# Optimization experiments

Hardware: AMD Instinct MI355X
Metric: run time of the kernel (lower is better)

Reference implementation:

```python
import jax, jax.numpy as jnp
import numpy as np

N, E, G = 50000, 640000, 256
NODE_IN, EDGE_IN, EXT_IN = 32, 16, 8
H, L = 128, 3
BN_EPS = 1e-5


def _linear_init(key, fan_in, fan_out):
    kw, kb = jax.random.split(key)
    s = 1.0 / np.sqrt(fan_in)
    w = jax.random.uniform(kw, (fan_in, fan_out), minval=-s, maxval=s, dtype=jnp.float32)
    b = jax.random.uniform(kb, (fan_out,), minval=-s, maxval=s, dtype=jnp.float32)
    return w, b


def setup_inputs() -> dict:
    key = jax.random.key(0)
    ks = jax.random.split(key, 16)
    x = jax.random.normal(ks[0], (N, NODE_IN), dtype=jnp.float32)
    edge_index = jax.random.randint(ks[1], (2, E), 0, N)
    edge_attr = jax.random.normal(ks[2], (E, EDGE_IN), dtype=jnp.float32)
    batch = jnp.sort(jax.random.randint(ks[3], (N,), 0, G))
    externals = jax.random.normal(ks[4], (G, EXT_IN), dtype=jnp.float32)

    node_w, node_b = _linear_init(ks[5], NODE_IN, H)
    ee_w1, ee_b1 = _linear_init(ks[6], EDGE_IN, H)
    ee_w2, ee_b2 = _linear_init(ks[7], H, H)
    # stacked per-layer GINEConv MLP params: [L, H, H] / [L, H]
    cks = jax.random.split(ks[8], 2 * L)
    cw1, cb1, cw2, cb2 = [], [], [], []
    for l in range(L):
        w1, b1 = _linear_init(cks[2 * l], H, H)
        w2, b2 = _linear_init(cks[2 * l + 1], H, H)
        cw1.append(w1); cb1.append(b1); cw2.append(w2); cb2.append(b2)
    conv_w1 = jnp.stack(cw1); conv_b1 = jnp.stack(cb1)
    conv_w2 = jnp.stack(cw2); conv_b2 = jnp.stack(cb2)
    bn_gamma = jnp.ones((L, H), dtype=jnp.float32)
    bn_beta = jnp.zeros((L, H), dtype=jnp.float32)
    ext_w1, ext_b1 = _linear_init(ks[9], EXT_IN, H)
    ext_w2, ext_b2 = _linear_init(ks[10], H, H)
    reg_w1, reg_b1 = _linear_init(ks[11], 2 * H, H)
    reg_w2, reg_b2 = _linear_init(ks[12], H, 1)

    return dict(x=x, edge_attr=edge_attr, externals=externals,
                node_w=node_w, node_b=node_b,
                ee_w1=ee_w1, ee_b1=ee_b1, ee_w2=ee_w2, ee_b2=ee_b2,
                conv_w1=conv_w1, conv_b1=conv_b1, conv_w2=conv_w2, conv_b2=conv_b2,
                bn_gamma=bn_gamma, bn_beta=bn_beta,
                ext_w1=ext_w1, ext_b1=ext_b1, ext_w2=ext_w2, ext_b2=ext_b2,
                reg_w1=reg_w1, reg_b1=reg_b1, reg_w2=reg_w2, reg_b2=reg_b2,
                edge_index=edge_index, batch=batch, num_graphs=G)


def reference(x, edge_attr, externals,
              node_w, node_b, ee_w1, ee_b1, ee_w2, ee_b2,
              conv_w1, conv_b1, conv_w2, conv_b2, bn_gamma, bn_beta,
              ext_w1, ext_b1, ext_w2, ext_b2,
              reg_w1, reg_b1, reg_w2, reg_b2,
              edge_index, batch, num_graphs):
    n = x.shape[0]
    src, dst = edge_index[0], edge_index[1]
    h = x @ node_w + node_b                                      # [N,H]
    e = jax.nn.relu(edge_attr @ ee_w1 + ee_b1) @ ee_w2 + ee_b2   # [E,H]
    for l in range(conv_w1.shape[0]):
        # GINEConv (eps=0): aggr = sum_j relu(x_j + e_ij); out = MLP(x_i + aggr)
        msg = jax.nn.relu(h[src] + e)                            # gather + add + relu [E,H]
        aggr = jax.ops.segment_sum(msg, dst, num_segments=n)     # scatter-add [N,H]
        z = h + aggr
        z = jax.nn.relu(z @ conv_w1[l] + conv_b1[l]) @ conv_w2[l] + conv_b2[l]
        # BatchNorm1d (batch statistics)
        mean = z.mean(axis=0)
        var = z.var(axis=0)
        z = (z - mean) * jax.lax.rsqrt(var + BN_EPS) * bn_gamma[l] + bn_beta[l]
        h = jax.nn.relu(z)                                       # dropout = identity (eval)
    # global mean pool over graphs
    gsum = jax.ops.segment_sum(h, batch, num_segments=num_graphs)
    cnt = jax.ops.segment_sum(jnp.ones((n, 1), h.dtype), batch, num_segments=num_graphs)
    graph_emb = gsum / jnp.maximum(cnt, 1.0)
    ext = jax.nn.relu(externals @ ext_w1 + ext_b1) @ ext_w2 + ext_b2
    comb = jnp.concatenate([graph_emb, ext], axis=-1)            # [G,2H]
    out = jax.nn.relu(comb @ reg_w1 + reg_b1) @ reg_w2 + reg_b2  # [G,1]
    return out.squeeze(-1)
```

## Files before the change

kernel.cpp:

```cpp
#include <hip/hip_runtime.h>

typedef __bf16 bf16_t;
typedef __bf16 bf16x8 __attribute__((ext_vector_type(8)));
typedef __bf16 bf16x4 __attribute__((ext_vector_type(4)));
typedef __bf16 bf16x2 __attribute__((ext_vector_type(2)));
typedef float  f32x4  __attribute__((ext_vector_type(4)));

#define MFMA16(a, b, c) __builtin_amdgcn_mfma_f32_16x16x32_bf16((a), (b), (c), 0, 0, 0)

__global__ __launch_bounds__(256) void prep_all_kernel(
    const float* __restrict__ nw,  const float* __restrict__ ew1,
    const float* __restrict__ ew2, const float* __restrict__ cw1,
    const float* __restrict__ cw2,
    bf16_t* __restrict__ nwt,  bf16_t* __restrict__ ew1t,
    bf16_t* __restrict__ ew2t, bf16_t* __restrict__ cw1t,
    bf16_t* __restrict__ cw2t)
{
    int b = blockIdx.x;
    const float* W; bf16_t* O; int Kact, KP, lb;
    if (b < 16)       { W = nw;  O = nwt;  Kact = 32;  KP = 32;  lb = b; }
    else if (b < 32)  { W = ew1; O = ew1t; Kact = 16;  KP = 32;  lb = b - 16; }
    else if (b < 96)  { W = ew2; O = ew2t; Kact = 128; KP = 128; lb = b - 32; }
    else if (b < 288) { int l = (b - 96) / 64;  W = cw1 + l * 16384; O = cw1t + l * 16384;
                        Kact = 128; KP = 128; lb = (b - 96) % 64; }
    else              { int l = (b - 288) / 64; W = cw2 + l * 16384; O = cw2t + l * 16384;
                        Kact = 128; KP = 128; lb = (b - 288) % 64; }
    int idx = lb * 256 + threadIdx.x;
    if (idx >= 128 * KP) return;
    int j    = idx & 7;
    int lane = (idx >> 3) & 63;
    int ct   = (idx >> 9) & 7;
    int kc   = idx >> 12;
    int n = ct * 16 + (lane & 15);
    int k = kc * 32 + (lane >> 4) * 8 + j;
    O[idx] = (bf16_t)((k < Kact) ? W[k * 128 + n] : 0.0f);
}

__global__ __launch_bounds__(256) void hist_kernel(const int* __restrict__ ei,
                                                   int* __restrict__ deg, int E,
                                                   const float* __restrict__ ea) {
    int t = blockIdx.x * 256 + threadIdx.x;
    if (t < E) {
        atomicAdd(&deg[ei[(long)E + t]], 1);
        float w0 = ea[(long)t * 16];
        float w1 = ea[(long)t * 16 + 8];
        asm volatile("" :: "v"(w0), "v"(w1));
    }
}

__global__ __launch_bounds__(256) void scanA_kernel(const int* __restrict__ deg,
                                                    int* __restrict__ partials,
                                                    int* __restrict__ bsums, int N) {
    __shared__ int s[256];
    int b = blockIdx.x, t = threadIdx.x;
    int base = b * 1024 + t * 4;
    int v0 = (base + 0 < N) ? deg[base + 0] : 0;
    int v1 = (base + 1 < N) ? deg[base + 1] : 0;
    int v2 = (base + 2 < N) ? deg[base + 2] : 0;
    int v3 = (base + 3 < N) ? deg[base + 3] : 0;
    int local = v0 + v1 + v2 + v3;
    s[t] = local;
    __syncthreads();
    for (int off = 1; off < 256; off <<= 1) {
        int v = (t >= off) ? s[t - off] : 0;
        __syncthreads();
        s[t] += v;
        __syncthreads();
    }
    int excl = s[t] - local;
    if (base + 0 < N) partials[base + 0] = excl;
    if (base + 1 < N) partials[base + 1] = excl + v0;
    if (base + 2 < N) partials[base + 2] = excl + v0 + v1;
    if (base + 3 < N) partials[base + 3] = excl + v0 + v1 + v2;
    if (t == 255) bsums[b] = s[255];
}

__global__ __launch_bounds__(256) void scanB_kernel(const int* __restrict__ bsums,
                                                    int* __restrict__ boff,
                                                    int* __restrict__ rowptr,
                                                    int NB, int N) {
    __shared__ int s[256];
    int t = threadIdx.x;
    int local = (t < NB) ? bsums[t] : 0;
    s[t] = local;
    __syncthreads();
    for (int off = 1; off < 256; off <<= 1) {
        int v = (t >= off) ? s[t - off] : 0;
        __syncthreads();
        s[t] += v;
        __syncthreads();
    }
    if (t < NB) boff[t] = s[t] - local;
    if (t == NB - 1) rowptr[N] = s[t];
}

__global__ __launch_bounds__(256) void scanC_kernel(const int* __restrict__ partials,
                                                    const int* __restrict__ boff,
                                                    int* __restrict__ rowptr,
                                                    int* __restrict__ cursor, int N) {
    int i = blockIdx.x * 256 + threadIdx.x;
    if (i >= N) return;
    int v = partials[i] + boff[i >> 10];
    rowptr[i] = v;
    cursor[i] = v;
}

__global__ __launch_bounds__(256) void scatter_kernel(const int* __restrict__ ei,
                                                      int* __restrict__ cursor,
                                                      int* __restrict__ srcp,
                                                      int* __restrict__ epos, int E) {
    int t = blockIdx.x * 256 + threadIdx.x;
    if (t >= E) return;
    int d = ei[(long)E + t];
    int pos = atomicAdd(&cursor[d], 1);
    srcp[pos] = ei[t];
    epos[t] = pos;
}

__global__ __launch_bounds__(256) void node_enc_kernel(
    const float* __restrict__ A, int M,
    const bf16_t* __restrict__ Ws, const float* __restrict__ bias,
    bf16_t* __restrict__ outp)
{
    constexpr int S = 136;
    __shared__ bf16_t T[128 * S];

    const int  tid  = threadIdx.x;
    const int  wv   = tid >> 6, lane = tid & 63;
    const long row0 = (long)blockIdx.x * 128;
    const int  l16  = lane & 15, quad = lane >> 4;

    {
        int r  = wv * 32 + (lane >> 1);
        long gr = row0 + r;
        int c0 = (lane & 1) * 16;
#pragma unroll
        for (int q = 0; q < 4; ++q) {
            float4 v = make_float4(0.f, 0.f, 0.f, 0.f);
            if (gr < M) v = *(const float4*)(A + gr * 32 + c0 + q * 4);
            bf16_t* d = &T[r * S + c0 + q * 4];
            d[0] = (bf16_t)v.x; d[1] = (bf16_t)v.y; d[2] = (bf16_t)v.z; d[3] = (bf16_t)v.w;
        }
    }

    f32x4 acc[2][8];
#pragma unroll
    for (int r = 0; r < 2; r++)
#pragma unroll
        for (int c = 0; c < 8; c++) acc[r][c] = (f32x4){0.f, 0.f, 0.f, 0.f};

    {
        bf16x8 af0 = *(const bf16x8*)&T[(wv * 32 + l16) * S + quad * 8];
        bf16x8 af1 = *(const bf16x8*)&T[(wv * 32 + 16 + l16) * S + quad * 8];
#pragma unroll
        for (int c = 0; c < 8; c++) {
            bf16x8 bfr = *(const bf16x8*)&Ws[((c * 64) + lane) * 8];
            acc[0][c] = MFMA16(af0, bfr, acc[0][c]);
            acc[1][c] = MFMA16(af1, bfr, acc[1][c]);
        }
    }

#pragma unroll
    for (int r = 0; r < 2; r++) {
        int mrow = wv * 32 + r * 16 + quad * 4;
#pragma unroll
        for (int c = 0; c < 8; c++) {
            int col = c * 16 + l16;
            float bb = bias[col];
#pragma unroll
            for (int q = 0; q < 4; q++)
                T[(mrow + q) * S + col] = (bf16_t)(acc[r][c][q] + bb);
        }
    }

#pragma unroll
    for (int it = 0; it < 8; ++it) {
        int idx = it * 64 + lane;
        int row = wv * 32 + (idx >> 4);
        int seg = idx & 15;
        long grow = row0 + row;
        if (grow < M)
            *(uint4*)&outp[grow * 128 + seg * 8] = *(const uint4*)&T[row * S + seg * 8];
    }
}

__global__ __launch_bounds__(256) void edge_mlp_kernel(
    const float* __restrict__ A, int M,
    const bf16_t* __restrict__ Ws1, const float* __restrict__ b1,
    const bf16_t* __restrict__ Ws2, const float* __restrict__ b2,
    const int* __restrict__ epos, bf16_t* __restrict__ outp)
{
    constexpr int S = 136;
    __shared__ bf16_t T[64 * S];

    const int  tid  = threadIdx.x;
    const int  wv   = tid >> 6, lane = tid & 63;
    const long row0 = (long)blockIdx.x * 64;
    const int  l16  = lane & 15, quad = lane >> 4;

    {
        int  r  = wv * 16 + (lane >> 2);
        long gr = row0 + r;
        float4 v = make_float4(0.f, 0.f, 0.f, 0.f);
        if (gr < M) v = *(const float4*)(A + gr * 16 + (lane & 3) * 4);
        bf16_t* d = &T[r * S + (lane & 3) * 4];
        d[0] = (bf16_t)v.x; d[1] = (bf16_t)v.y; d[2] = (bf16_t)v.z; d[3] = (bf16_t)v.w;
    }

    f32x4 acc[8];
#pragma unroll
    for (int c = 0; c < 8; c++) acc[c] = (f32x4){0.f, 0.f, 0.f, 0.f};

    {
        bf16x8 af;
#pragma unroll
        for (int j = 0; j < 8; ++j) af[j] = (bf16_t)0.f;
        if (quad < 2) af = *(const bf16x8*)&T[(wv * 16 + l16) * S + quad * 8];
#pragma unroll
        for (int c = 0; c < 8; c++) {
            bf16x8 bfr = *(const bf16x8*)&Ws1[((c * 64) + lane) * 8];
            acc[c] = MFMA16(af, bfr, acc[c]);
        }
    }

    const int mbase = wv * 16 + quad * 4;

#pragma unroll
    for (int c = 0; c < 8; c++) {
        int col = c * 16 + l16;
        float bb = b1[col];
#pragma unroll
        for (int q = 0; q < 4; q++)
            T[(mbase + q) * S + col] = (bf16_t)fmaxf(acc[c][q] + bb, 0.f);
    }

#pragma unroll
    for (int c = 0; c < 8; c++) acc[c] = (f32x4){0.f, 0.f, 0.f, 0.f};

#pragma unroll
    for (int kc = 0; kc < 4; ++kc) {
        bf16x8 af = *(const bf16x8*)&T[(wv * 16 + l16) * S + kc * 32 + quad * 8];
#pragma unroll
        for (int c = 0; c < 8; c++) {
            bf16x8 bfr = *(const bf16x8*)&Ws2[(((kc * 8 + c) * 64) + lane) * 8];
            acc[c] = MFMA16(af, bfr, acc[c]);
        }
    }

#pragma unroll
    for (int c = 0; c < 8; c++) {
        int col = c * 16 + l16;
        float bb = b2[col];
#pragma unroll
        for (int q = 0; q < 4; q++)
            T[(mbase + q) * S + col] = (bf16_t)(acc[c][q] + bb);
    }

#pragma unroll
    for (int it = 0; it < 4; ++it) {
        int idx = it * 64 + lane;
        int row = wv * 16 + (idx >> 4);
        int seg = idx & 15;
        long grow = row0 + row;
        if (grow < M) {
            long pos = epos[grow];
            *(uint4*)&outp[pos * 128 + seg * 8] = *(const uint4*)&T[row * S + seg * 8];
        }
    }
}

__global__ __launch_bounds__(256) void bnx_kernel(
    const bf16_t* __restrict__ z, const float* __restrict__ bns,
    const float* __restrict__ gamma, const float* __restrict__ beta,
    bf16_t* __restrict__ hbuf, int N)
{
    long t = (long)blockIdx.x * 256 + threadIdx.x;
    long i0 = t * 8;
    if (i0 >= (long)N * 128) return;
    int c = (int)(i0 & 127);
    const float invN = 1.f / (float)N;
    bf16x8 v = *(const bf16x8*)(z + i0);
    bf16x8 o;
#pragma unroll
    for (int u = 0; u < 8; ++u) {
        int cc = c + u;
        float m  = bns[cc] * invN;
        float va = bns[128 + cc] * invN - m * m;
        float iv = rsqrtf(va + 1e-5f);
        float sc = gamma[cc] * iv;
        float sh = beta[cc] - m * sc;
        o[u] = (bf16_t)fmaxf((float)v[u] * sc + sh, 0.f);
    }
    *(bf16x8*)(hbuf + i0) = o;
}

__global__ __launch_bounds__(512, 8) void aggr_conv_kernel(
    const bf16_t* __restrict__ xin,
    const bf16_t* __restrict__ e,
    const int* __restrict__ rowptr, const int* __restrict__ srcp, int M,
    const bf16_t* __restrict__ Ws1, const float* __restrict__ b1,
    const bf16_t* __restrict__ Ws2, const float* __restrict__ b2,
    bf16_t* __restrict__ zout, float* __restrict__ bn_out)
{
    constexpr int S = 136;
    __shared__ bf16_t T[32 * S];
    __shared__ float  wred[2][256];

    const int  tid  = threadIdx.x;
    const int  wv   = tid >> 6, lane = tid & 63;
    const long row0 = (long)blockIdx.x * 32;
    const int  l16  = lane & 15, quad = lane >> 4;

    const long nbase = row0 + wv * 4;
    int rpv = 0;
    {
        long idx = nbase + lane;
        if (idx > M) idx = M;
        if (lane <= 4) rpv = rowptr[idx];
    }

#pragma unroll 1
    for (int ri = 0; ri < 4; ++ri) {
        const int  r   = wv * 4 + ri;
        const long n   = row0 + r;
        const int  beg = __shfl(rpv, ri);
        const int  end = __shfl(rpv, ri + 1);
        float ax = 0.f, ay = 0.f;
        if (n < M) {
            bf16x2 xv = *(const bf16x2*)(xin + n * 128 + lane * 2);
            ax = (float)xv[0]; ay = (float)xv[1];
            for (int base = beg; base < end; base += 64) {
                int cnt = min(64, end - base);
                int sv  = (base + lane < end) ? srcp[base + lane] : 0;
                int j = 0;
                for (; j + 3 < cnt; j += 4) {
                    int s0 = __shfl(sv, j),     s1 = __shfl(sv, j + 1);
                    int s2 = __shfl(sv, j + 2), s3 = __shfl(sv, j + 3);
                    bf16x2 x0 = *(const bf16x2*)(xin + (long)s0 * 128 + lane * 2);
                    bf16x2 x1 = *(const bf16x2*)(xin + (long)s1 * 128 + lane * 2);
                    bf16x2 x2 = *(const bf16x2*)(xin + (long)s2 * 128 + lane * 2);
                    bf16x2 x3 = *(const bf16x2*)(xin + (long)s3 * 128 + lane * 2);
                    bf16x2 e0 = *(const bf16x2*)(e + (long)(base + j + 0) * 128 + lane * 2);
                    bf16x2 e1 = *(const bf16x2*)(e + (long)(base + j + 1) * 128 + lane * 2);
                    bf16x2 e2 = *(const bf16x2*)(e + (long)(base + j + 2) * 128 + lane * 2);
                    bf16x2 e3 = *(const bf16x2*)(e + (long)(base + j + 3) * 128 + lane * 2);
                    ax += fmaxf((float)x0[0] + (float)e0[0], 0.f);
                    ay += fmaxf((float)x0[1] + (float)e0[1], 0.f);
                    ax += fmaxf((float)x1[0] + (float)e1[0], 0.f);
                    ay += fmaxf((float)x1[1] + (float)e1[1], 0.f);
                    ax += fmaxf((float)x2[0] + (float)e2[0], 0.f);
                    ay += fmaxf((float)x2[1] + (float)e2[1], 0.f);
                    ax += fmaxf((float)x3[0] + (float)e3[0], 0.f);
                    ay += fmaxf((float)x3[1] + (float)e3[1], 0.f);
                }
                for (; j < cnt; ++j) {
                    int s0 = __shfl(sv, j);
                    bf16x2 x0 = *(const bf16x2*)(xin + (long)s0 * 128 + lane * 2);
                    bf16x2 e0 = *(const bf16x2*)(e + (long)(base + j) * 128 + lane * 2);
                    ax += fmaxf((float)x0[0] + (float)e0[0], 0.f);
                    ay += fmaxf((float)x0[1] + (float)e0[1], 0.f);
                }
            }
        }
        bf16x2 o; o[0] = (bf16_t)ax; o[1] = (bf16_t)ay;
        *(bf16x2*)&T[r * S + lane * 2] = o;
    }
    __syncthreads();

    const int rb = wv >> 2, cq = wv & 3;
    const int mbase = rb * 16 + quad * 4;

    f32x4 acc[2];
#pragma unroll
    for (int c = 0; c < 2; c++) acc[c] = (f32x4){0.f, 0.f, 0.f, 0.f};

#pragma unroll
    for (int kc = 0; kc < 4; ++kc) {
        bf16x8 af = *(const bf16x8*)&T[(rb * 16 + l16) * S + kc * 32 + quad * 8];
#pragma unroll
        for (int c = 0; c < 2; c++) {
            int ct = cq * 2 + c;
            bf16x8 bfr = *(const bf16x8*)&Ws1[(((kc * 8 + ct) * 64) + lane) * 8];
            acc[c] = MFMA16(af, bfr, acc[c]);
        }
    }
    __syncthreads();

#pragma unroll
    for (int c = 0; c < 2; c++) {
        int col = (cq * 2 + c) * 16 + l16;
        float bb = b1[col];
#pragma unroll
        for (int q = 0; q < 4; q++)
            T[(mbase + q) * S + col] = (bf16_t)fmaxf(acc[c][q] + bb, 0.f);
    }
    __syncthreads();

#pragma unroll
    for (int c = 0; c < 2; c++) acc[c] = (f32x4){0.f, 0.f, 0.f, 0.f};

#pragma unroll
    for (int kc = 0; kc < 4; ++kc) {
        bf16x8 af = *(const bf16x8*)&T[(rb * 16 + l16) * S + kc * 32 + quad * 8];
#pragma unroll
        for (int c = 0; c < 2; c++) {
            int ct = cq * 2 + c;
            bf16x8 bfr = *(const bf16x8*)&Ws2[(((kc * 8 + ct) * 64) + lane) * 8];
            acc[c] = MFMA16(af, bfr, acc[c]);
        }
    }
    __syncthreads();

#pragma unroll
    for (int c = 0; c < 2; c++) {
        int col = (cq * 2 + c) * 16 + l16;
        float bb = b2[col];
        float s = 0.f, s2 = 0.f;
#pragma unroll
        for (int q = 0; q < 4; q++) {
            float v = acc[c][q] + bb;
            T[(mbase + q) * S + col] = (bf16_t)v;
            if (row0 + mbase + q < M) { s += v; s2 += v * v; }
        }
        s  += __shfl_xor(s, 16);  s  += __shfl_xor(s, 32);
        s2 += __shfl_xor(s2, 16); s2 += __shfl_xor(s2, 32);
        if (quad == 0) {
            wred[rb][col]       = s;
            wred[rb][128 + col] = s2;
        }
    }
    __syncthreads();

    {
        int row = tid >> 4, seg = tid & 15;
        long grow = row0 + row;
        if (grow < M)
            *(uint4*)&zout[grow * 128 + seg * 8] = *(const uint4*)&T[row * S + seg * 8];
    }
    if (tid < 256) {
        float v = wred[0][tid] + wred[1][tid];
        atomicAdd(&bn_out[tid], v);
    }
}

__global__ __launch_bounds__(128) void pool_kernel(
    const bf16_t* __restrict__ z, const float* __restrict__ bns,
    const float* __restrict__ gamma, const float* __restrict__ beta,
    const int* __restrict__ batch,
    float* __restrict__ gsum, float* __restrict__ cnt, int N)
{
    int c = threadIdx.x;
    float mean = bns[c] / (float)N;
    float var  = bns[128 + c] / (float)N - mean * mean;
    float inv  = rsqrtf(var + 1e-5f);
    float sc   = gamma[c] * inv;
    float sh   = beta[c] - mean * sc;
    int n0 = blockIdx.x * 32;
    int n1 = min(n0 + 32, N);
    float acc = 0.f;
    int cur = -1, rc = 0;
    for (int n = n0; n < n1; ++n) {
        int g = batch[n];
        if (g != cur) {
            if (cur >= 0) {
                atomicAdd(&gsum[(long)cur * 128 + c], acc);
                if (c == 0) atomicAdd(&cnt[cur], (float)rc);
            }
            cur = g; acc = 0.f; rc = 0;
        }
        acc += fmaxf((float)z[(long)n * 128 + c] * sc + sh, 0.f);
        rc++;
    }
    if (cur >= 0) {
        atomicAdd(&gsum[(long)cur * 128 + c], acc);
        if (c == 0) atomicAdd(&cnt[cur], (float)rc);
    }
}

__global__ __launch_bounds__(128) void head_kernel(
    const float* __restrict__ gsum, const float* __restrict__ cnt,
    const float* __restrict__ ext_in,
    const float* __restrict__ ew1, const float* __restrict__ eb1,
    const float* __restrict__ ew2, const float* __restrict__ eb2,
    const float* __restrict__ rw1, const float* __restrict__ rb1,
    const float* __restrict__ rw2, const float* __restrict__ rb2,
    float* __restrict__ out)
{
    int g = blockIdx.x, c = threadIdx.x;
    __shared__ float sx[8];
    __shared__ float h1[128];
    __shared__ float comb[256];
    __shared__ float red[128];

    if (c < 8) sx[c] = ext_in[g * 8 + c];
    __syncthreads();
    float a = eb1[c];
#pragma unroll
    for (int k = 0; k < 8; k++) a += sx[k] * ew1[k * 128 + c];
    h1[c] = fmaxf(a, 0.f);
    __syncthreads();
    float b = eb2[c];
    for (int k = 0; k < 128; k++) b += h1[k] * ew2[k * 128 + c];
    comb[c]       = gsum[(long)g * 128 + c] / fmaxf(cnt[g], 1.0f);
    comb[128 + c] = b;
    __syncthreads();
    float r = rb1[c];
    for (int k = 0; k < 256; k++) r += comb[k] * rw1[k * 128 + c];
    r = fmaxf(r, 0.f);
    red[c] = r * rw2[c];
    __syncthreads();
    if (c == 0) {
        float s = rb2[0];
        for (int k = 0; k < 128; k++) s += red[k];
        out[g] = s;
    }
}

extern "C" void kernel_launch(void* const* d_in, const int* in_sizes, int n_in,
                              void* d_out, int out_size, void* d_ws, size_t ws_size,
                              hipStream_t stream)
{
    const float* x         = (const float*)d_in[0];
    const float* edge_attr = (const float*)d_in[1];
    const float* externals = (const float*)d_in[2];
    const float* node_w    = (const float*)d_in[3];
    const float* node_b    = (const float*)d_in[4];
    const float* ee_w1     = (const float*)d_in[5];
    const float* ee_b1     = (const float*)d_in[6];
    const float* ee_w2     = (const float*)d_in[7];
    const float* ee_b2     = (const float*)d_in[8];
    const float* conv_w1   = (const float*)d_in[9];
    const float* conv_b1   = (const float*)d_in[10];
    const float* conv_w2   = (const float*)d_in[11];
    const float* conv_b2   = (const float*)d_in[12];
    const float* bn_gamma  = (const float*)d_in[13];
    const float* bn_beta   = (const float*)d_in[14];
    const float* ext_w1    = (const float*)d_in[15];
    const float* ext_b1    = (const float*)d_in[16];
    const float* ext_w2    = (const float*)d_in[17];
    const float* ext_b2    = (const float*)d_in[18];
    const float* reg_w1    = (const float*)d_in[19];
    const float* reg_b1    = (const float*)d_in[20];
    const float* reg_w2    = (const float*)d_in[21];
    const float* reg_b2    = (const float*)d_in[22];
    const int* edge_index  = (const int*)d_in[23];
    const int* batch       = (const int*)d_in[24];

    const int N = in_sizes[0] / 32;
    const int E = in_sizes[1] / 16;
    const int G = in_sizes[2] / 8;
    const int NB = (N + 1023) / 1024;

    char* p = (char*)d_ws;
    auto alloc = [&](size_t bytes) -> void* {
        void* r = (void*)p;
        p += (bytes + 255) & ~(size_t)255;
        return r;
    };
    bf16_t* h       = (bf16_t*)alloc((size_t)N * 128 * 2);
    bf16_t* zA      = (bf16_t*)alloc((size_t)N * 128 * 2);
    bf16_t* zB      = (bf16_t*)alloc((size_t)N * 128 * 2);
    bf16_t* hb      = (bf16_t*)alloc((size_t)N * 128 * 2);
    bf16_t* ebuf    = (bf16_t*)alloc((size_t)E * 128 * 2);
    int*    deg     = (int*)alloc((size_t)N * 4);
    int*    rowptr  = (int*)alloc(((size_t)N + 1) * 4);
    int*    cursor  = (int*)alloc((size_t)N * 4);
    int*    partials= (int*)alloc((size_t)N * 4);
    int*    bsums   = (int*)alloc((size_t)NB * 4);
    int*    boff    = (int*)alloc((size_t)NB * 4);
    int*    srcp    = (int*)alloc((size_t)E * 4);
    int*    epos    = (int*)alloc((size_t)E * 4);
    bf16_t* node_wt = (bf16_t*)alloc(128 * 32 * 2);
    bf16_t* ee_w1t  = (bf16_t*)alloc(128 * 32 * 2);
    bf16_t* ee_w2t  = (bf16_t*)alloc(128 * 128 * 2);
    bf16_t* cw1t    = (bf16_t*)alloc(3 * 128 * 128 * 2);
    bf16_t* cw2t    = (bf16_t*)alloc(3 * 128 * 128 * 2);
    float*  bns     = (float*)alloc(3 * 256 * 4);
    float*  gsum    = (float*)alloc((size_t)G * 128 * 4);
    float*  cnt     = (float*)alloc((size_t)G * 4);

    hipMemsetAsync(deg, 0, (size_t)N * 4, stream);
    hipMemsetAsync(bns, 0, 3 * 256 * 4, stream);
    hist_kernel<<<(E + 255) / 256, 256, 0, stream>>>(edge_index, deg, E, edge_attr);
    scanA_kernel<<<NB, 256, 0, stream>>>(deg, partials, bsums, N);
    scanB_kernel<<<1, 256, 0, stream>>>(bsums, boff, rowptr, NB, N);
    scanC_kernel<<<(N + 255) / 256, 256, 0, stream>>>(partials, boff, rowptr, cursor, N);
    scatter_kernel<<<(E + 255) / 256, 256, 0, stream>>>(edge_index, cursor, srcp, epos, E);

    prep_all_kernel<<<480, 256, 0, stream>>>(node_w, ee_w1, ee_w2, conv_w1, conv_w2,
                                             node_wt, ee_w1t, ee_w2t, cw1t, cw2t);

    node_enc_kernel<<<(N + 127) / 128, 256, 0, stream>>>(x, N, node_wt, node_b, h);

    edge_mlp_kernel<<<(E + 63) / 64, 256, 0, stream>>>(
        edge_attr, E, ee_w1t, ee_b1, ee_w2t, ee_b2, epos, ebuf);

    const int nblk = (N + 31) / 32;
    const int bblk = ((N * 128 / 8) + 255) / 256;
    aggr_conv_kernel<<<nblk, 512, 0, stream>>>(
        h, ebuf, rowptr, srcp, N,
        cw1t + 0 * 16384, conv_b1 + 0 * 128, cw2t + 0 * 16384, conv_b2 + 0 * 128,
        zA, bns + 0);
    bnx_kernel<<<bblk, 256, 0, stream>>>(zA, bns + 0, bn_gamma + 0, bn_beta + 0, hb, N);
    aggr_conv_kernel<<<nblk, 512, 0, stream>>>(
        hb, ebuf, rowptr, srcp, N,
        cw1t + 1 * 16384, conv_b1 + 1 * 128, cw2t + 1 * 16384, conv_b2 + 1 * 128,
        zB, bns + 256);
    bnx_kernel<<<bblk, 256, 0, stream>>>(zB, bns + 256, bn_gamma + 128, bn_beta + 128, hb, N);
    aggr_conv_kernel<<<nblk, 512, 0, stream>>>(
        hb, ebuf, rowptr, srcp, N,
        cw1t + 2 * 16384, conv_b1 + 2 * 128, cw2t + 2 * 16384, conv_b2 + 2 * 128,
        zA, bns + 512);

    hipMemsetAsync(gsum, 0, (size_t)G * 128 * 4, stream);
    hipMemsetAsync(cnt, 0, (size_t)G * 4, stream);
    pool_kernel<<<(N + 31) / 32, 128, 0, stream>>>(zA, bns + 512, bn_gamma + 256, bn_beta + 256,
                                                   batch, gsum, cnt, N);
    head_kernel<<<G, 128, 0, stream>>>(gsum, cnt, externals,
                                       ext_w1, ext_b1, ext_w2, ext_b2,
                                       reg_w1, reg_b1, reg_w2, reg_b2,
                                       (float*)d_out);
}
```

Measured before the change: 549.5 us.

## Stage edge features via async global-to-LDS loads and batch 16 neighbor gathers

Result: slower. 594.7 us (+8.2%).

```diff
diff --git a/kernel.cpp b/kernel.cpp
--- a/kernel.cpp
+++ b/kernel.cpp
@@ -7,6 +7,9 @@
 typedef float  f32x4  __attribute__((ext_vector_type(4)));
 
 #define MFMA16(a, b, c) __builtin_amdgcn_mfma_f32_16x16x32_bf16((a), (b), (c), 0, 0, 0)
+
+typedef __attribute__((address_space(1))) const void gvoid_t;
+typedef __attribute__((address_space(3))) void svoid_t;
 
 __global__ __launch_bounds__(256) void prep_all_kernel(
     const float* __restrict__ nw,  const float* __restrict__ ew1,
@@ -294,7 +297,7 @@
     *(bf16x8*)(hbuf + i0) = o;
 }
 
-__global__ __launch_bounds__(512, 8) void aggr_conv_kernel(
+__global__ __launch_bounds__(512, 6) void aggr_conv_kernel(
     const bf16_t* __restrict__ xin,
     const bf16_t* __restrict__ e,
     const int* __restrict__ rowptr, const int* __restrict__ srcp, int M,
@@ -305,11 +308,14 @@
     constexpr int S = 136;
     __shared__ bf16_t T[32 * S];
     __shared__ float  wred[2][256];
+    __shared__ bf16_t Elds[8][16 * 128];
 
     const int  tid  = threadIdx.x;
     const int  wv   = tid >> 6, lane = tid & 63;
     const long row0 = (long)blockIdx.x * 32;
     const int  l16  = lane & 15, quad = lane >> 4;
+
+    bf16_t* eslot = &Elds[wv][0];
 
     const long nbase = row0 + wv * 4;
     int rpv = 0;
@@ -327,39 +333,51 @@
         const int  end = __shfl(rpv, ri + 1);
         float ax = 0.f, ay = 0.f;
         if (n < M) {
-            bf16x2 xv = *(const bf16x2*)(xin + n * 128 + lane * 2);
-            ax = (float)xv[0]; ay = (float)xv[1];
-            for (int base = beg; base < end; base += 64) {
-                int cnt = min(64, end - base);
-                int sv  = (base + lane < end) ? srcp[base + lane] : 0;
-                int j = 0;
-                for (; j + 3 < cnt; j += 4) {
-                    int s0 = __shfl(sv, j),     s1 = __shfl(sv, j + 1);
-                    int s2 = __shfl(sv, j + 2), s3 = __shfl(sv, j + 3);
-                    bf16x2 x0 = *(const bf16x2*)(xin + (long)s0 * 128 + lane * 2);
-                    bf16x2 x1 = *(const bf16x2*)(xin + (long)s1 * 128 + lane * 2);
-                    bf16x2 x2 = *(const bf16x2*)(xin + (long)s2 * 128 + lane * 2);
-                    bf16x2 x3 = *(const bf16x2*)(xin + (long)s3 * 128 + lane * 2);
-                    bf16x2 e0 = *(const bf16x2*)(e + (long)(base + j + 0) * 128 + lane * 2);
-                    bf16x2 e1 = *(const bf16x2*)(e + (long)(base + j + 1) * 128 + lane * 2);
-                    bf16x2 e2 = *(const bf16x2*)(e + (long)(base + j + 2) * 128 + lane * 2);
-                    bf16x2 e3 = *(const bf16x2*)(e + (long)(base + j + 3) * 128 + lane * 2);
-                    ax += fmaxf((float)x0[0] + (float)e0[0], 0.f);
-                    ay += fmaxf((float)x0[1] + (float)e0[1], 0.f);
-                    ax += fmaxf((float)x1[0] + (float)e1[0], 0.f);
-                    ay += fmaxf((float)x1[1] + (float)e1[1], 0.f);
-                    ax += fmaxf((float)x2[0] + (float)e2[0], 0.f);
-                    ay += fmaxf((float)x2[1] + (float)e2[1], 0.f);
-                    ax += fmaxf((float)x3[0] + (float)e3[0], 0.f);
-                    ay += fmaxf((float)x3[1] + (float)e3[1], 0.f);
+            bf16x2 xv0 = *(const bf16x2*)(xin + n * 128 + lane * 2);
+            ax = (float)xv0[0]; ay = (float)xv0[1];
+#pragma unroll 1
+            for (int base = beg; base < end; base += 16) {
+                int cnt = min(16, end - base);
+#pragma unroll
+                for (int i = 0; i < 4; ++i) {
+                    __builtin_amdgcn_global_load_lds(
+                        (gvoid_t*)(e + (long)base * 128 + i * 512 + lane * 8),
+                        (svoid_t*)(eslot + i * 512),
+                        16, 0, 0);
                 }
-                for (; j < cnt; ++j) {
-                    int s0 = __shfl(sv, j);
-                    bf16x2 x0 = *(const bf16x2*)(xin + (long)s0 * 128 + lane * 2);
-                    bf16x2 e0 = *(const bf16x2*)(e + (long)(base + j) * 128 + lane * 2);
-                    ax += fmaxf((float)x0[0] + (float)e0[0], 0.f);
-                    ay += fmaxf((float)x0[1] + (float)e0[1], 0.f);
-                }
+                int sv = (lane < 16 && base + lane < end) ? srcp[base + lane] : 0;
+                bf16x2 xr0  = *(const bf16x2*)(xin + (long)__shfl(sv, 0)  * 128 + lane * 2);
+                bf16x2 xr1  = *(const bf16x2*)(xin + (long)__shfl(sv, 1)  * 128 + lane * 2);
+                bf16x2 xr2  = *(const bf16x2*)(xin + (long)__shfl(sv, 2)  * 128 + lane * 2);
+                bf16x2 xr3  = *(const bf16x2*)(xin + (long)__shfl(sv, 3)  * 128 + lane * 2);
+                bf16x2 xr4  = *(const bf16x2*)(xin + (long)__shfl(sv, 4)  * 128 + lane * 2);
+                bf16x2 xr5  = *(const bf16x2*)(xin + (long)__shfl(sv, 5)  * 128 + lane * 2);
+                bf16x2 xr6  = *(const bf16x2*)(xin + (long)__shfl(sv, 6)  * 128 + lane * 2);
+                bf16x2 xr7  = *(const bf16x2*)(xin + (long)__shfl(sv, 7)  * 128 + lane * 2);
+                bf16x2 xr8  = *(const bf16x2*)(xin + (long)__shfl(sv, 8)  * 128 + lane * 2);
+                bf16x2 xr9  = *(const bf16x2*)(xin + (long)__shfl(sv, 9)  * 128 + lane * 2);
+                bf16x2 xr10 = *(const bf16x2*)(xin + (long)__shfl(sv, 10) * 128 + lane * 2);
+                bf16x2 xr11 = *(const bf16x2*)(xin + (long)__shfl(sv, 11) * 128 + lane * 2);
+                bf16x2 xr12 = *(const bf16x2*)(xin + (long)__shfl(sv, 12) * 128 + lane * 2);
+                bf16x2 xr13 = *(const bf16x2*)(xin + (long)__shfl(sv, 13) * 128 + lane * 2);
+                bf16x2 xr14 = *(const bf16x2*)(xin + (long)__shfl(sv, 14) * 128 + lane * 2);
+                bf16x2 xr15 = *(const bf16x2*)(xin + (long)__shfl(sv, 15) * 128 + lane * 2);
+                asm volatile("s_waitcnt vmcnt(0)" ::: "memory");
+                __builtin_amdgcn_sched_barrier(0);
+#define ACC_E(J, XR)                                                           \
+                do {                                                           \
+                    if (J < cnt) {                                             \
+                        bf16x2 ev = *(const bf16x2*)(eslot + J * 128 + lane * 2); \
+                        ax += fmaxf((float)XR[0] + (float)ev[0], 0.f);         \
+                        ay += fmaxf((float)XR[1] + (float)ev[1], 0.f);         \
+                    }                                                          \
+                } while (0)
+                ACC_E(0, xr0);   ACC_E(1, xr1);   ACC_E(2, xr2);   ACC_E(3, xr3);
+                ACC_E(4, xr4);   ACC_E(5, xr5);   ACC_E(6, xr6);   ACC_E(7, xr7);
+                ACC_E(8, xr8);   ACC_E(9, xr9);   ACC_E(10, xr10); ACC_E(11, xr11);
+                ACC_E(12, xr12); ACC_E(13, xr13); ACC_E(14, xr14); ACC_E(15, xr15);
+#undef ACC_E
+                __builtin_amdgcn_sched_barrier(0);
             }
         }
         bf16x2 o; o[0] = (bf16_t)ax; o[1] = (bf16_t)ay;
@@ -561,7 +579,7 @@
     bf16_t* zA      = (bf16_t*)alloc((size_t)N * 128 * 2);
     bf16_t* zB      = (bf16_t*)alloc((size_t)N * 128 * 2);
     bf16_t* hb      = (bf16_t*)alloc((size_t)N * 128 * 2);
-    bf16_t* ebuf    = (bf16_t*)alloc((size_t)E * 128 * 2);
+    bf16_t* ebuf    = (bf16_t*)alloc((size_t)E * 128 * 2 + 8192);
     int*    deg     = (int*)alloc((size_t)N * 4);
     int*    rowptr  = (int*)alloc(((size_t)N + 1) * 4);
     int*    cursor  = (int*)alloc((size_t)N * 4);
```

## Recompute edge MLP inside aggregation kernels instead of materializing edge embeddings

Applied to the files above, without the earlier changes.

Result: slower. 2.081 ms (+278.8%).

```diff
diff --git a/kernel.cpp b/kernel.cpp
--- a/kernel.cpp
+++ b/kernel.cpp
@@ -108,13 +108,18 @@
 __global__ __launch_bounds__(256) void scatter_kernel(const int* __restrict__ ei,
                                                       int* __restrict__ cursor,
                                                       int* __restrict__ srcp,
-                                                      int* __restrict__ epos, int E) {
+                                                      const float* __restrict__ ea,
+                                                      bf16_t* __restrict__ eac, int E) {
     int t = blockIdx.x * 256 + threadIdx.x;
     if (t >= E) return;
     int d = ei[(long)E + t];
     int pos = atomicAdd(&cursor[d], 1);
     srcp[pos] = ei[t];
-    epos[t] = pos;
+    bf16_t tmp[16];
+#pragma unroll
+    for (int k = 0; k < 16; ++k) tmp[k] = (bf16_t)ea[(long)t * 16 + k];
+    *(uint4*)(eac + (long)pos * 16)     = *(uint4*)(tmp);
+    *(uint4*)(eac + (long)pos * 16 + 8) = *(uint4*)(tmp + 8);
 }
 
 __global__ __launch_bounds__(256) void node_enc_kernel(
@@ -181,91 +186,6 @@
         long grow = row0 + row;
         if (grow < M)
             *(uint4*)&outp[grow * 128 + seg * 8] = *(const uint4*)&T[row * S + seg * 8];
-    }
-}
-
-__global__ __launch_bounds__(256) void edge_mlp_kernel(
-    const float* __restrict__ A, int M,
-    const bf16_t* __restrict__ Ws1, const float* __restrict__ b1,
-    const bf16_t* __restrict__ Ws2, const float* __restrict__ b2,
-    const int* __restrict__ epos, bf16_t* __restrict__ outp)
-{
-    constexpr int S = 136;
-    __shared__ bf16_t T[64 * S];
-
-    const int  tid  = threadIdx.x;
-    const int  wv   = tid >> 6, lane = tid & 63;
-    const long row0 = (long)blockIdx.x * 64;
-    const int  l16  = lane & 15, quad = lane >> 4;
-
-    {
-        int  r  = wv * 16 + (lane >> 2);
-        long gr = row0 + r;
-        float4 v = make_float4(0.f, 0.f, 0.f, 0.f);
-        if (gr < M) v = *(const float4*)(A + gr * 16 + (lane & 3) * 4);
-        bf16_t* d = &T[r * S + (lane & 3) * 4];
-        d[0] = (bf16_t)v.x; d[1] = (bf16_t)v.y; d[2] = (bf16_t)v.z; d[3] = (bf16_t)v.w;
-    }
-
-    f32x4 acc[8];
-#pragma unroll
-    for (int c = 0; c < 8; c++) acc[c] = (f32x4){0.f, 0.f, 0.f, 0.f};
-
-    {
-        bf16x8 af;
-#pragma unroll
-        for (int j = 0; j < 8; ++j) af[j] = (bf16_t)0.f;
-        if (quad < 2) af = *(const bf16x8*)&T[(wv * 16 + l16) * S + quad * 8];
-#pragma unroll
-        for (int c = 0; c < 8; c++) {
-            bf16x8 bfr = *(const bf16x8*)&Ws1[((c * 64) + lane) * 8];
-            acc[c] = MFMA16(af, bfr, acc[c]);
-        }
-    }
-
-    const int mbase = wv * 16 + quad * 4;
-
-#pragma unroll
-    for (int c = 0; c < 8; c++) {
-        int col = c * 16 + l16;
-        float bb = b1[col];
-#pragma unroll
-        for (int q = 0; q < 4; q++)
-            T[(mbase + q) * S + col] = (bf16_t)fmaxf(acc[c][q] + bb, 0.f);
-    }
-
-#pragma unroll
-    for (int c = 0; c < 8; c++) acc[c] = (f32x4){0.f, 0.f, 0.f, 0.f};
-
-#pragma unroll
-    for (int kc = 0; kc < 4; ++kc) {
-        bf16x8 af = *(const bf16x8*)&T[(wv * 16 + l16) * S + kc * 32 + quad * 8];
-#pragma unroll
-        for (int c = 0; c < 8; c++) {
-            bf16x8 bfr = *(const bf16x8*)&Ws2[(((kc * 8 + c) * 64) + lane) * 8];
-            acc[c] = MFMA16(af, bfr, acc[c]);
-        }
-    }
-
-#pragma unroll
-    for (int c = 0; c < 8; c++) {
-        int col = c * 16 + l16;
-        float bb = b2[col];
-#pragma unroll
-        for (int q = 0; q < 4; q++)
-            T[(mbase + q) * S + col] = (bf16_t)(acc[c][q] + bb);
-    }
-
-#pragma unroll
-    for (int it = 0; it < 4; ++it) {
-        int idx = it * 64 + lane;
-        int row = wv * 16 + (idx >> 4);
-        int seg = idx & 15;
-        long grow = row0 + row;
-        if (grow < M) {
-            long pos = epos[grow];
-            *(uint4*)&outp[pos * 128 + seg * 8] = *(const uint4*)&T[row * S + seg * 8];
-        }
     }
 }
 
@@ -296,79 +216,146 @@
 
 __global__ __launch_bounds__(512, 8) void aggr_conv_kernel(
     const bf16_t* __restrict__ xin,
-    const bf16_t* __restrict__ e,
+    const bf16_t* __restrict__ eac,
     const int* __restrict__ rowptr, const int* __restrict__ srcp, int M,
+    const bf16_t* __restrict__ We1, const float* __restrict__ be1,
+    const bf16_t* __restrict__ We2, const float* __restrict__ be2,
     const bf16_t* __restrict__ Ws1, const float* __restrict__ b1,
     const bf16_t* __restrict__ Ws2, const float* __restrict__ b2,
     bf16_t* __restrict__ zout, float* __restrict__ bn_out)
 {
     constexpr int S = 136;
-    __shared__ bf16_t T[32 * S];
+    constexpr int STe = 24;
+    __shared__ bf16_t Th[64 * S];
+    __shared__ bf16_t Te[64 * STe];
+    __shared__ float  Acc[32 * 128];
     __shared__ float  wred[2][256];
+    __shared__ int    rptile[33];
+    __shared__ int    dloc[64];
+    __shared__ int    sloc[64];
 
     const int  tid  = threadIdx.x;
     const int  wv   = tid >> 6, lane = tid & 63;
     const long row0 = (long)blockIdx.x * 32;
     const int  l16  = lane & 15, quad = lane >> 4;
 
-    const long nbase = row0 + wv * 4;
-    int rpv = 0;
+    if (tid <= 32) {
+        long idx = row0 + tid;
+        if (idx > M) idx = M;
+        rptile[tid] = rowptr[idx];
+    }
     {
-        long idx = nbase + lane;
-        if (idx > M) idx = M;
-        if (lane <= 4) rpv = rowptr[idx];
-    }
+        int row = tid >> 4;
+        int c0  = (tid & 15) * 8;
+        long n  = row0 + row;
+        if (n < M) {
+            bf16x8 xv = *(const bf16x8*)(xin + n * 128 + c0);
+#pragma unroll
+            for (int u = 0; u < 8; ++u) Acc[row * 128 + c0 + u] = (float)xv[u];
+        } else {
+#pragma unroll
+            for (int u = 0; u < 8; ++u) Acc[row * 128 + c0 + u] = 0.f;
+        }
+    }
+    __syncthreads();
+
+    const int eb = rptile[0];
+    const int ee = rptile[32];
+
+    const int rg = wv >> 1, ch = wv & 1;
+    const int mbase = rg * 16 + quad * 4;
 
 #pragma unroll 1
-    for (int ri = 0; ri < 4; ++ri) {
-        const int  r   = wv * 4 + ri;
-        const long n   = row0 + r;
-        const int  beg = __shfl(rpv, ri);
-        const int  end = __shfl(rpv, ri + 1);
-        float ax = 0.f, ay = 0.f;
-        if (n < M) {
-            bf16x2 xv = *(const bf16x2*)(xin + n * 128 + lane * 2);
-            ax = (float)xv[0]; ay = (float)xv[1];
-            for (int base = beg; base < end; base += 64) {
-                int cnt = min(64, end - base);
-                int sv  = (base + lane < end) ? srcp[base + lane] : 0;
-                int j = 0;
-                for (; j + 3 < cnt; j += 4) {
-                    int s0 = __shfl(sv, j),     s1 = __shfl(sv, j + 1);
-                    int s2 = __shfl(sv, j + 2), s3 = __shfl(sv, j + 3);
-                    bf16x2 x0 = *(const bf16x2*)(xin + (long)s0 * 128 + lane * 2);
-                    bf16x2 x1 = *(const bf16x2*)(xin + (long)s1 * 128 + lane * 2);
-                    bf16x2 x2 = *(const bf16x2*)(xin + (long)s2 * 128 + lane * 2);
-                    bf16x2 x3 = *(const bf16x2*)(xin + (long)s3 * 128 + lane * 2);
-                    bf16x2 e0 = *(const bf16x2*)(e + (long)(base + j + 0) * 128 + lane * 2);
-                    bf16x2 e1 = *(const bf16x2*)(e + (long)(base + j + 1) * 128 + lane * 2);
-                    bf16x2 e2 = *(const bf16x2*)(e + (long)(base + j + 2) * 128 + lane * 2);
-                    bf16x2 e3 = *(const bf16x2*)(e + (long)(base + j + 3) * 128 + lane * 2);
-                    ax += fmaxf((float)x0[0] + (float)e0[0], 0.f);
-                    ay += fmaxf((float)x0[1] + (float)e0[1], 0.f);
-                    ax += fmaxf((float)x1[0] + (float)e1[0], 0.f);
-                    ay += fmaxf((float)x1[1] + (float)e1[1], 0.f);
-                    ax += fmaxf((float)x2[0] + (float)e2[0], 0.f);
-                    ay += fmaxf((float)x2[1] + (float)e2[1], 0.f);
-                    ax += fmaxf((float)x3[0] + (float)e3[0], 0.f);
-                    ay += fmaxf((float)x3[1] + (float)e3[1], 0.f);
-                }
-                for (; j < cnt; ++j) {
-                    int s0 = __shfl(sv, j);
-                    bf16x2 x0 = *(const bf16x2*)(xin + (long)s0 * 128 + lane * 2);
-                    bf16x2 e0 = *(const bf16x2*)(e + (long)(base + j) * 128 + lane * 2);
-                    ax += fmaxf((float)x0[0] + (float)e0[0], 0.f);
-                    ay += fmaxf((float)x0[1] + (float)e0[1], 0.f);
+    for (int cb = eb; cb < ee; cb += 64) {
+        const int cc = min(64, ee - cb);
+        if (tid < 256) {
+            int row = tid >> 2, c4 = (tid & 3) * 4;
+            bf16x4 v = (bf16x4){(bf16_t)0.f, (bf16_t)0.f, (bf16_t)0.f, (bf16_t)0.f};
+            if (row < cc) v = *(const bf16x4*)(eac + (long)(cb + row) * 16 + c4);
+            *(bf16x4*)&Te[row * STe + c4] = v;
+        }
+        if (tid < 64) {
+            sloc[tid] = (tid < cc) ? srcp[cb + tid] : 0;
+            int target = cb + tid;
+            int i = 0;
+#pragma unroll
+            for (int step = 16; step; step >>= 1)
+                if (i + step <= 31 && rptile[i + step] <= target) i += step;
+            dloc[tid] = i;
+        }
+        __syncthreads();
+
+        f32x4 a1[4];
+#pragma unroll
+        for (int ct = 0; ct < 4; ++ct) a1[ct] = (f32x4){0.f, 0.f, 0.f, 0.f};
+        {
+            bf16x8 af;
+#pragma unroll
+            for (int j = 0; j < 8; ++j) af[j] = (bf16_t)0.f;
+            if (quad < 2) af = *(const bf16x8*)&Te[(rg * 16 + l16) * STe + quad * 8];
+#pragma unroll
+            for (int ct = 0; ct < 4; ++ct) {
+                bf16x8 bfr = *(const bf16x8*)&We1[(((ch * 4 + ct) * 64) + lane) * 8];
+                a1[ct] = MFMA16(af, bfr, a1[ct]);
+            }
+        }
+        __syncthreads();
+#pragma unroll
+        for (int ct = 0; ct < 4; ++ct) {
+            int col = (ch * 4 + ct) * 16 + l16;
+            float bb = be1[col];
+#pragma unroll
+            for (int q = 0; q < 4; q++)
+                Th[(mbase + q) * S + col] = (bf16_t)fmaxf(a1[ct][q] + bb, 0.f);
+        }
+        __syncthreads();
+
+        f32x4 a2[4];
+#pragma unroll
+        for (int ct = 0; ct < 4; ++ct) a2[ct] = (f32x4){0.f, 0.f, 0.f, 0.f};
+#pragma unroll
+        for (int kc = 0; kc < 4; ++kc) {
+            bf16x8 af = *(const bf16x8*)&Th[(rg * 16 + l16) * S + kc * 32 + quad * 8];
+#pragma unroll
+            for (int ct = 0; ct < 4; ++ct) {
+                bf16x8 bfr = *(const bf16x8*)&We2[(((kc * 8 + ch * 4 + ct) * 64) + lane) * 8];
+                a2[ct] = MFMA16(af, bfr, a2[ct]);
+            }
+        }
+#pragma unroll
+        for (int ct = 0; ct < 4; ++ct) {
+            int col = (ch * 4 + ct) * 16 + l16;
+            float be = be2[col];
+            float hv[4];
+#pragma unroll
+            for (int q = 0; q < 4; q++) {
+                int sr = sloc[mbase + q];
+                hv[q] = (float)xin[(long)sr * 128 + col];
+            }
+#pragma unroll
+            for (int q = 0; q < 4; q++) {
+                int row = mbase + q;
+                if (row < cc) {
+                    float m = fmaxf(hv[q] + a2[ct][q] + be, 0.f);
+                    atomicAdd(&Acc[dloc[row] * 128 + col], m);
                 }
             }
         }
-        bf16x2 o; o[0] = (bf16_t)ax; o[1] = (bf16_t)ay;
-        *(bf16x2*)&T[r * S + lane * 2] = o;
+        __syncthreads();
+    }
+
+    {
+        int row = tid >> 4;
+        int c0  = (tid & 15) * 8;
+        bf16x8 o;
+#pragma unroll
+        for (int u = 0; u < 8; ++u) o[u] = (bf16_t)Acc[row * 128 + c0 + u];
+        *(uint4*)&Th[row * S + c0] = *(uint4*)&o;
     }
     __syncthreads();
 
     const int rb = wv >> 2, cq = wv & 3;
-    const int mbase = rb * 16 + quad * 4;
+    const int cmb = rb * 16 + quad * 4;
 
     f32x4 acc[2];
 #pragma unroll
@@ -376,7 +363,7 @@
 
 #pragma unroll
     for (int kc = 0; kc < 4; ++kc) {
-        bf16x8 af = *(const bf16x8*)&T[(rb * 16 + l16) * S + kc * 32 + quad * 8];
+        bf16x8 af = *(const bf16x8*)&Th[(rb * 16 + l16) * S + kc * 32 + quad * 8];
 #pragma unroll
         for (int c = 0; c < 2; c++) {
             int ct = cq * 2 + c;
@@ -392,7 +379,7 @@
         float bb = b1[col];
 #pragma unroll
         for (int q = 0; q < 4; q++)
-            T[(mbase + q) * S + col] = (bf16_t)fmaxf(acc[c][q] + bb, 0.f);
+            Th[(cmb + q) * S + col] = (bf16_t)fmaxf(acc[c][q] + bb, 0.f);
     }
     __syncthreads();
 
@@ -401,7 +388,7 @@
 
 #pragma unroll
     for (int kc = 0; kc < 4; ++kc) {
-        bf16x8 af = *(const bf16x8*)&T[(rb * 16 + l16) * S + kc * 32 + quad * 8];
+        bf16x8 af = *(const bf16x8*)&Th[(rb * 16 + l16) * S + kc * 32 + quad * 8];
 #pragma unroll
         for (int c = 0; c < 2; c++) {
             int ct = cq * 2 + c;
@@ -419,8 +406,8 @@
 #pragma unroll
         for (int q = 0; q < 4; q++) {
             float v = acc[c][q] + bb;
-            T[(mbase + q) * S + col] = (bf16_t)v;
-            if (row0 + mbase + q < M) { s += v; s2 += v * v; }
+            Th[(cmb + q) * S + col] = (bf16_t)v;
+            if (row0 + cmb + q < M) { s += v; s2 += v * v; }
         }
         s  += __shfl_xor(s, 16);  s  += __shfl_xor(s, 32);
         s2 += __shfl_xor(s2, 16); s2 += __shfl_xor(s2, 32);
@@ -435,7 +422,7 @@
         int row = tid >> 4, seg = tid & 15;
         long grow = row0 + row;
         if (grow < M)
-            *(uint4*)&zout[grow * 128 + seg * 8] = *(const uint4*)&T[row * S + seg * 8];
+            *(uint4*)&zout[grow * 128 + seg * 8] = *(const uint4*)&Th[row * S + seg * 8];
     }
     if (tid < 256) {
         float v = wred[0][tid] + wred[1][tid];
@@ -561,7 +548,7 @@
     bf16_t* zA      = (bf16_t*)alloc((size_t)N * 128 * 2);
     bf16_t* zB      = (bf16_t*)alloc((size_t)N * 128 * 2);
     bf16_t* hb      = (bf16_t*)alloc((size_t)N * 128 * 2);
-    bf16_t* ebuf    = (bf16_t*)alloc((size_t)E * 128 * 2);
+    bf16_t* eac     = (bf16_t*)alloc((size_t)E * 16 * 2);
     int*    deg     = (int*)alloc((size_t)N * 4);
     int*    rowptr  = (int*)alloc(((size_t)N + 1) * 4);
     int*    cursor  = (int*)alloc((size_t)N * 4);
@@ -569,7 +556,6 @@
     int*    bsums   = (int*)alloc((size_t)NB * 4);
     int*    boff    = (int*)alloc((size_t)NB * 4);
     int*    srcp    = (int*)alloc((size_t)E * 4);
-    int*    epos    = (int*)alloc((size_t)E * 4);
     bf16_t* node_wt = (bf16_t*)alloc(128 * 32 * 2);
     bf16_t* ee_w1t  = (bf16_t*)alloc(128 * 32 * 2);
     bf16_t* ee_w2t  = (bf16_t*)alloc(128 * 128 * 2);
@@ -585,30 +571,31 @@
     scanA_kernel<<<NB, 256, 0, stream>>>(deg, partials, bsums, N);
     scanB_kernel<<<1, 256, 0, stream>>>(bsums, boff, rowptr, NB, N);
     scanC_kernel<<<(N + 255) / 256, 256, 0, stream>>>(partials, boff, rowptr, cursor, N);
-    scatter_kernel<<<(E + 255) / 256, 256, 0, stream>>>(edge_index, cursor, srcp, epos, E);
+    scatter_kernel<<<(E + 255) / 256, 256, 0, stream>>>(edge_index, cursor, srcp,
+                                                        edge_attr, eac, E);
 
     prep_all_kernel<<<480, 256, 0, stream>>>(node_w, ee_w1, ee_w2, conv_w1, conv_w2,
                                              node_wt, ee_w1t, ee_w2t, cw1t, cw2t);
 
     node_enc_kernel<<<(N + 127) / 128, 256, 0, stream>>>(x, N, node_wt, node_b, h);
-
-    edge_mlp_kernel<<<(E + 63) / 64, 256, 0, stream>>>(
-        edge_attr, E, ee_w1t, ee_b1, ee_w2t, ee_b2, epos, ebuf);
 
     const int nblk = (N + 31) / 32;
     const int bblk = ((N * 128 / 8) + 255) / 256;
     aggr_conv_kernel<<<nblk, 512, 0, stream>>>(
-        h, ebuf, rowptr, srcp, N,
+        h, eac, rowptr, srcp, N,
+        ee_w1t, ee_b1, ee_w2t, ee_b2,
         cw1t + 0 * 16384, conv_b1 + 0 * 128, cw2t + 0 * 16384, conv_b2 + 0 * 128,
         zA, bns + 0);
     bnx_kernel<<<bblk, 256, 0, stream>>>(zA, bns + 0, bn_gamma + 0, bn_beta + 0, hb, N);
     aggr_conv_kernel<<<nblk, 512, 0, stream>>>(
-        hb, ebuf, rowptr, srcp, N,
+        hb, eac, rowptr, srcp, N,
+        ee_w1t, ee_b1, ee_w2t, ee_b2,
         cw1t + 1 * 16384, conv_b1 + 1 * 128, cw2t + 1 * 16384, conv_b2 + 1 * 128,
         zB, bns + 256);
     bnx_kernel<<<bblk, 256, 0, stream>>>(zB, bns + 256, bn_gamma + 128, bn_beta + 128, hb, N);
     aggr_conv_kernel<<<nblk, 512, 0, stream>>>(
-        hb, ebuf, rowptr, srcp, N,
+        hb, eac, rowptr, srcp, N,
+        ee_w1t, ee_b1, ee_w2t, ee_b2,
         cw1t + 2 * 16384, conv_b1 + 2 * 128, cw2t + 2 * 16384, conv_b2 + 2 * 128,
         zA, bns + 512);
 
```
